# Performance work log

Hardware: AMD Instinct MI355X
Metric: run time of the kernel (lower is better)

The kernel has to match this reference:

```python
import jax, jax.numpy as jnp
import numpy as np

N_PROBLEMS = 20000
N_SKILLS = 1000
EMB_SIZE = 128
TIME_LOG = 5.0
B, L = 64, 1024


def setup_inputs() -> dict:
    key = jax.random.key(0)
    ks = jax.random.split(key, 10)
    skills = jax.random.randint(ks[0], (B, L), 0, N_SKILLS)
    problems = jax.random.randint(ks[1], (B, L), 0, N_PROBLEMS)
    labels = jax.random.randint(ks[2], (B, L), 0, 2)
    times = jnp.sort(jax.random.randint(ks[3], (B, L), 0, 1_000_000), axis=-1)
    inp = jnp.stack([skills, problems, labels, times], axis=1)  # [B,4,L]
    std = 0.01
    return {
        "input": inp,
        "problem_base": std * jax.random.normal(ks[4], (N_PROBLEMS, 1), jnp.float32),
        "skill_base": std * jax.random.normal(ks[5], (N_SKILLS, 1), jnp.float32),
        "alpha_inter": std * jax.random.normal(ks[6], (N_SKILLS * 2, EMB_SIZE), jnp.float32),
        "alpha_skill": std * jax.random.normal(ks[7], (N_SKILLS, EMB_SIZE), jnp.float32),
        "beta_inter": std * jax.random.normal(ks[8], (N_SKILLS * 2, EMB_SIZE), jnp.float32),
        "beta_skill": std * jax.random.normal(ks[9], (N_SKILLS, EMB_SIZE), jnp.float32),
    }


def reference(input, problem_base, skill_base, alpha_inter, alpha_skill, beta_inter, beta_skill):
    skills = input[:, 0]    # [B,L]
    problems = input[:, 1]
    labels = input[:, 2]
    times = input[:, 3]

    mask_labels = labels * (labels < 2).astype(labels.dtype)
    inters = skills + mask_labels * N_SKILLS  # [B,L] in [0, 2*N_SKILLS)

    # pairwise Hawkes excitation / decay scores: [B,L,L]
    alphas = jnp.einsum('bie,bje->bij', alpha_inter[inters], alpha_skill[skills])
    betas = jnp.einsum('bie,bje->bij', beta_inter[inters], beta_skill[skills])
    betas = jnp.clip(betas + 1.0, 0.0, 10.0)

    dt = jnp.abs(times[:, :, None] - times[:, None, :]).astype(jnp.float32)
    log_dt = jnp.log(dt + 1e-10) / np.log(TIME_LOG)

    cross_effects = alphas * jnp.exp(-betas * log_dt)

    seq_len = skills.shape[1]
    # keep strictly-upper-triangular entries (source i before target j)
    keep = jnp.triu(jnp.ones((seq_len, seq_len), dtype=bool), k=1)
    sum_t = jnp.where(keep[None], cross_effects, 0.0).sum(axis=-2)  # [B,L]

    problem_bias = problem_base[problems][..., 0]
    skill_bias = skill_base[skills][..., 0]
    return jax.nn.sigmoid(problem_bias + skill_bias + sum_t)
```

## Files before the change

### kernel.cpp

```cpp
#include <hip/hip_runtime.h>
#include <hip/hip_bf16.h>

#define NB   64
#define SL   1024
#define EMB  128
#define NSK  1000
#define TJ   64
#define TI   64
#define SB   136
#define NS   4

#define AI_OFF 0
#define BI_OFF 256000
#define AS_OFF 512000
#define BS_OFF 640000
#define TB_ELEMS 768000
#define ACC_BYTE_OFF (TB_ELEMS * 2)
#define ACC_ELEMS (NS * NB * SL)

using short8  = __attribute__((ext_vector_type(8))) short;
using floatx4 = __attribute__((ext_vector_type(4))) float;

__device__ inline unsigned cvt2(float x, float y) {
    float2 f; f.x = x; f.y = y;
    __hip_bfloat162 h = __float22bfloat162_rn(f);
    unsigned u; __builtin_memcpy(&u, &h, sizeof(u));
    return u;
}

extern "C" __global__ __launch_bounds__(256)
void cvt_tables(const float* __restrict__ ai, const float* __restrict__ bi,
                const float* __restrict__ as, const float* __restrict__ bs,
                unsigned short* __restrict__ dst)
{
    const int t = blockIdx.x * 256 + threadIdx.x;
    const long e = (long)t * 8;
    const float* src;
    if      (e < 256000) src = ai + e;
    else if (e < 512000) src = bi + (e - 256000);
    else if (e < 640000) src = as + (e - 512000);
    else                 src = bs + (e - 640000);
    float4 f0 = *(const float4*)src;
    float4 f1 = *(const float4*)(src + 4);
    uint4 pk;
    pk.x = cvt2(f0.x, f0.y); pk.y = cvt2(f0.z, f0.w);
    pk.z = cvt2(f1.x, f1.y); pk.w = cvt2(f1.z, f1.w);
    *(uint4*)(dst + e) = pk;
}

__device__ __noinline__ float fixup_pair(const float* __restrict__ air,
                                         const float* __restrict__ bir,
                                         const float* __restrict__ asr,
                                         const float* __restrict__ bsr) {
    float da = 0.f, db = 0.f;
    for (int k = 0; k < EMB; ++k) {
        da += air[k] * asr[k];
        db += bir[k] * bsr[k];
    }
    float beta = fminf(fmaxf(db + 1.f, 0.f), 10.f);
    return da * __expf(beta * 14.30676558073393f);
}

extern "C" __global__ __launch_bounds__(256)
void hawkes_main(const int*   __restrict__ inp,
                 const float* __restrict__ ainter,
                 const float* __restrict__ askill,
                 const float* __restrict__ bint,
                 const float* __restrict__ bsk,
                 const unsigned short* __restrict__ tb,
                 float*       __restrict__ acc)
{
    __shared__ unsigned short lA[2][TI][SB];

    const int bid  = blockIdx.x;
    const int b    = bid & (NB - 1);
    const int r    = bid >> 6;
    const int jt   = (SL / TJ - 1) - ((r >> 2) & 15);
    const int s    = r & 3;
    const int tid  = threadIdx.x;
    const int w    = tid >> 6;
    const int l    = tid & 63;
    const int quad = l >> 4;
    const int col  = l & 15;

    const int* __restrict__ binp = inp + b * 4 * SL;

    const int jlane = jt * TJ + w * 16 + col;
    const int sk_j  = binp[jlane];
    const int tj    = binp[3 * SL + jlane];
    const float* asr = askill + (long)sk_j * EMB;
    const float* bsr = bsk    + (long)sk_j * EMB;

    const unsigned short* asr16 = tb + AS_OFF + (long)sk_j * EMB;
    const unsigned short* bsr16 = tb + BS_OFF + (long)sk_j * EMB;
    short8 bfa[4], bfb[4];
#pragma unroll
    for (int ks = 0; ks < 4; ++ks) {
        int k0 = ks * 32 + quad * 8;
        bfa[ks] = *(const short8*)(asr16 + k0);
        bfb[ks] = *(const short8*)(bsr16 + k0);
    }

    float sum = 0.f;

    const int srow = tid >> 2;
    const int sq   = tid & 3;

    for (int it = s; it <= jt; it += NS) {
        const int itb = it * TI;

        {
            const int irow  = itb + srow;
            const int ski   = binp[irow];
            const int li    = binp[2 * SL + irow];
            const long intr = ski + (long)li * NSK;
            const unsigned short* sA = tb + AI_OFF + intr * EMB + sq * 32;
            const unsigned short* sBm = tb + BI_OFF + intr * EMB + sq * 32;
            uint4 a0 = *(const uint4*)(sA);
            uint4 a1 = *(const uint4*)(sA + 8);
            uint4 a2 = *(const uint4*)(sA + 16);
            uint4 a3 = *(const uint4*)(sA + 24);
            uint4 b0 = *(const uint4*)(sBm);
            uint4 b1 = *(const uint4*)(sBm + 8);
            uint4 b2 = *(const uint4*)(sBm + 16);
            uint4 b3 = *(const uint4*)(sBm + 24);
            unsigned short* dA = &lA[0][srow][sq * 32];
            unsigned short* dB = &lA[1][srow][sq * 32];
            *(uint4*)(dA)      = a0;
            *(uint4*)(dA + 8)  = a1;
            *(uint4*)(dA + 16) = a2;
            *(uint4*)(dA + 24) = a3;
            *(uint4*)(dB)      = b0;
            *(uint4*)(dB + 8)  = b1;
            *(uint4*)(dB + 16) = b2;
            *(uint4*)(dB + 24) = b3;
        }
        __syncthreads();

#pragma unroll
        for (int isub = 0; isub < 4; ++isub) {
            floatx4 acca = {0.f, 0.f, 0.f, 0.f};
            floatx4 accb = {0.f, 0.f, 0.f, 0.f};
#pragma unroll
            for (int ks = 0; ks < 4; ++ks) {
                int k0 = ks * 32 + quad * 8;
                short8 av = *(const short8*)&lA[0][isub * 16 + col][k0];
                short8 bv = *(const short8*)&lA[1][isub * 16 + col][k0];
                acca = __builtin_amdgcn_mfma_f32_16x16x32_bf16(av, bfa[ks], acca, 0, 0, 0);
                accb = __builtin_amdgcn_mfma_f32_16x16x32_bf16(bv, bfb[ks], accb, 0, 0, 0);
            }
            const int ibase = itb + isub * 16 + quad * 4;
            const int4 t4 = *(const int4*)(binp + 3 * SL + ibase);
#pragma unroll
            for (int rr = 0; rr < 4; ++rr) {
                const int iidx = ibase + rr;
                if (iidx < jlane) {
                    const int ti = (rr == 0) ? t4.x : (rr == 1) ? t4.y : (rr == 2) ? t4.z : t4.w;
                    const int dt = tj - ti;
                    if (dt != 0) {
                        float beta = fminf(fmaxf(accb[rr] + 1.f, 0.f), 10.f);
                        float lc   = __log2f((float)dt) * 0.43067655807339306f;
                        sum += acca[rr] * exp2f(-beta * lc);
                    } else {
                        const int ski   = binp[iidx];
                        const int li    = binp[2 * SL + iidx];
                        const long intr = ski + (long)li * NSK;
                        sum += fixup_pair(ainter + intr * EMB, bint + intr * EMB, asr, bsr);
                    }
                }
            }
        }
        __syncthreads();
    }

    sum += __shfl_xor(sum, 16, 64);
    sum += __shfl_xor(sum, 32, 64);

    if (quad == 0) {
        acc[(((long)s * NB + b) << 10) + jlane] = sum;
    }
}

extern "C" __global__ __launch_bounds__(256)
void hawkes_finalize(const int* __restrict__ inp, const float* __restrict__ pbase,
                     const float* __restrict__ sbase, const float* __restrict__ acc,
                     float* __restrict__ out)
{
    const int t = blockIdx.x * 256 + threadIdx.x;
    const int b = t >> 10, j = t & (SL - 1);
    const int* binp = inp + b * 4 * SL;
    float sum = acc[t] + acc[NB * SL + t] + acc[2 * NB * SL + t] + acc[3 * NB * SL + t];
    const float x = pbase[binp[SL + j]] + sbase[binp[j]] + sum;
    out[t] = 1.f / (1.f + __expf(-x));
}

extern "C" void kernel_launch(void* const* d_in, const int* in_sizes, int n_in,
                              void* d_out, int out_size, void* d_ws, size_t ws_size,
                              hipStream_t stream) {
    const int*   inp = (const int*)d_in[0];
    const float* pb  = (const float*)d_in[1];
    const float* sb  = (const float*)d_in[2];
    const float* ai  = (const float*)d_in[3];
    const float* as  = (const float*)d_in[4];
    const float* bi  = (const float*)d_in[5];
    const float* bs  = (const float*)d_in[6];

    unsigned short* tb  = (unsigned short*)d_ws;
    float*          acc = (float*)((char*)d_ws + ACC_BYTE_OFF);

    cvt_tables<<<dim3(96000 / 256), dim3(256), 0, stream>>>(ai, bi, as, bs, tb);
    hawkes_main<<<dim3(NB * (SL / TJ) * NS), dim3(256), 0, stream>>>(
        inp, ai, as, bi, bs, tb, acc);
    hawkes_finalize<<<dim3(NB * SL / 256), dim3(256), 0, stream>>>(
        inp, pb, sb, acc, (float*)d_out);
}
```

Baseline: 131.6 us.

## Swap loop order: stage i-tile once in LDS, stream 128-wide j-tiles

Each block now loads one 64-row i-tile of interaction embeddings into shared memory once and loops over 128-column j-tiles. Each wave handles two 16-column j groups, so every LDS read feeds four MFMAs instead of two. The loop-internal barriers and per-tile reloads go away. Partial sums are written per i-tile and reduced in a variable-length loop in the finalize kernel. In exchange, the j-side skill fragments are reloaded from global memory for every j-tile, register pressure rises, and the accumulator buffer grows to 16 slices.

```diff
diff --git a/kernel.cpp b/kernel.cpp
--- a/kernel.cpp
+++ b/kernel.cpp
@@ -5,10 +5,9 @@
 #define SL   1024
 #define EMB  128
 #define NSK  1000
-#define TJ   64
 #define TI   64
 #define SB   136
-#define NS   4
+#define NS   2
 
 #define AI_OFF 0
 #define BI_OFF 256000
@@ -16,10 +15,11 @@
 #define BS_OFF 640000
 #define TB_ELEMS 768000
 #define ACC_BYTE_OFF (TB_ELEMS * 2)
-#define ACC_ELEMS (NS * NB * SL)
 
 using short8  = __attribute__((ext_vector_type(8))) short;
 using floatx4 = __attribute__((ext_vector_type(4))) float;
+
+#define INV_LN5 0.6213349345596119f
 
 __device__ inline unsigned cvt2(float x, float y) {
     float2 f; f.x = x; f.y = y;
@@ -75,8 +75,8 @@
     const int bid  = blockIdx.x;
     const int b    = bid & (NB - 1);
     const int r    = bid >> 6;
-    const int jt   = (SL / TJ - 1) - ((r >> 2) & 15);
-    const int s    = r & 3;
+    const int it   = r >> 1;
+    const int s    = r & 1;
     const int tid  = threadIdx.x;
     const int w    = tid >> 6;
     const int l    = tid & 63;
@@ -84,100 +84,119 @@
     const int col  = l & 15;
 
     const int* __restrict__ binp = inp + b * 4 * SL;
-
-    const int jlane = jt * TJ + w * 16 + col;
-    const int sk_j  = binp[jlane];
-    const int tj    = binp[3 * SL + jlane];
-    const float* asr = askill + (long)sk_j * EMB;
-    const float* bsr = bsk    + (long)sk_j * EMB;
-
-    const unsigned short* asr16 = tb + AS_OFF + (long)sk_j * EMB;
-    const unsigned short* bsr16 = tb + BS_OFF + (long)sk_j * EMB;
-    short8 bfa[4], bfb[4];
-#pragma unroll
-    for (int ks = 0; ks < 4; ++ks) {
-        int k0 = ks * 32 + quad * 8;
-        bfa[ks] = *(const short8*)(asr16 + k0);
-        bfb[ks] = *(const short8*)(bsr16 + k0);
+    const int itb = it * TI;
+
+    {
+        const int srow  = tid >> 2;
+        const int sq    = tid & 3;
+        const int irow  = itb + srow;
+        const int ski   = binp[irow];
+        const int li    = binp[2 * SL + irow];
+        const long intr = ski + (long)li * NSK;
+        const unsigned short* sA  = tb + AI_OFF + intr * EMB + sq * 32;
+        const unsigned short* sBm = tb + BI_OFF + intr * EMB + sq * 32;
+        uint4 a0 = *(const uint4*)(sA);
+        uint4 a1 = *(const uint4*)(sA + 8);
+        uint4 a2 = *(const uint4*)(sA + 16);
+        uint4 a3 = *(const uint4*)(sA + 24);
+        uint4 b0 = *(const uint4*)(sBm);
+        uint4 b1 = *(const uint4*)(sBm + 8);
+        uint4 b2 = *(const uint4*)(sBm + 16);
+        uint4 b3 = *(const uint4*)(sBm + 24);
+        unsigned short* dA = &lA[0][srow][sq * 32];
+        unsigned short* dB = &lA[1][srow][sq * 32];
+        *(uint4*)(dA)      = a0; *(uint4*)(dA + 8)  = a1;
+        *(uint4*)(dA + 16) = a2; *(uint4*)(dA + 24) = a3;
+        *(uint4*)(dB)      = b0; *(uint4*)(dB + 8)  = b1;
+        *(uint4*)(dB + 16) = b2; *(uint4*)(dB + 24) = b3;
     }
 
-    float sum = 0.f;
-
-    const int srow = tid >> 2;
-    const int sq   = tid & 3;
-
-    for (int it = s; it <= jt; it += NS) {
-        const int itb = it * TI;
-
+    int4 t4s[4];
+#pragma unroll
+    for (int isub = 0; isub < 4; ++isub)
+        t4s[isub] = *(const int4*)(binp + 3 * SL + itb + isub * 16 + quad * 4);
+
+    __syncthreads();
+
+    const int jt_min = it >> 1;
+    for (int jt = jt_min; jt < 8; ++jt) {
+        if ((jt & 1) != s) continue;
+        const int jbase = jt * 128 + w * 32;
+        const int j0 = jbase + col;
+        const int j1 = jbase + 16 + col;
+        const int sk0 = binp[j0],        sk1 = binp[j1];
+        const int tj0 = binp[3*SL + j0], tj1 = binp[3*SL + j1];
+
+        short8 f00[4], f01[4], f10[4], f11[4];
         {
-            const int irow  = itb + srow;
-            const int ski   = binp[irow];
-            const int li    = binp[2 * SL + irow];
-            const long intr = ski + (long)li * NSK;
-            const unsigned short* sA = tb + AI_OFF + intr * EMB + sq * 32;
-            const unsigned short* sBm = tb + BI_OFF + intr * EMB + sq * 32;
-            uint4 a0 = *(const uint4*)(sA);
-            uint4 a1 = *(const uint4*)(sA + 8);
-            uint4 a2 = *(const uint4*)(sA + 16);
-            uint4 a3 = *(const uint4*)(sA + 24);
-            uint4 b0 = *(const uint4*)(sBm);
-            uint4 b1 = *(const uint4*)(sBm + 8);
-            uint4 b2 = *(const uint4*)(sBm + 16);
-            uint4 b3 = *(const uint4*)(sBm + 24);
-            unsigned short* dA = &lA[0][srow][sq * 32];
-            unsigned short* dB = &lA[1][srow][sq * 32];
-            *(uint4*)(dA)      = a0;
-            *(uint4*)(dA + 8)  = a1;
-            *(uint4*)(dA + 16) = a2;
-            *(uint4*)(dA + 24) = a3;
-            *(uint4*)(dB)      = b0;
-            *(uint4*)(dB + 8)  = b1;
-            *(uint4*)(dB + 16) = b2;
-            *(uint4*)(dB + 24) = b3;
+            const unsigned short* p00 = tb + AS_OFF + (long)sk0 * EMB + quad * 8;
+            const unsigned short* p01 = tb + BS_OFF + (long)sk0 * EMB + quad * 8;
+            const unsigned short* p10 = tb + AS_OFF + (long)sk1 * EMB + quad * 8;
+            const unsigned short* p11 = tb + BS_OFF + (long)sk1 * EMB + quad * 8;
+#pragma unroll
+            for (int ks = 0; ks < 4; ++ks) {
+                f00[ks] = *(const short8*)(p00 + ks * 32);
+                f01[ks] = *(const short8*)(p01 + ks * 32);
+                f10[ks] = *(const short8*)(p10 + ks * 32);
+                f11[ks] = *(const short8*)(p11 + ks * 32);
+            }
         }
-        __syncthreads();
-
+
+        float sum0 = 0.f, sum1 = 0.f;
 #pragma unroll
         for (int isub = 0; isub < 4; ++isub) {
-            floatx4 acca = {0.f, 0.f, 0.f, 0.f};
-            floatx4 accb = {0.f, 0.f, 0.f, 0.f};
+            floatx4 aa0 = {0.f,0.f,0.f,0.f}, aa1 = {0.f,0.f,0.f,0.f};
+            floatx4 bb0 = {0.f,0.f,0.f,0.f}, bb1 = {0.f,0.f,0.f,0.f};
 #pragma unroll
             for (int ks = 0; ks < 4; ++ks) {
-                int k0 = ks * 32 + quad * 8;
+                const int k0 = ks * 32 + quad * 8;
                 short8 av = *(const short8*)&lA[0][isub * 16 + col][k0];
                 short8 bv = *(const short8*)&lA[1][isub * 16 + col][k0];
-                acca = __builtin_amdgcn_mfma_f32_16x16x32_bf16(av, bfa[ks], acca, 0, 0, 0);
-                accb = __builtin_amdgcn_mfma_f32_16x16x32_bf16(bv, bfb[ks], accb, 0, 0, 0);
+                aa0 = __builtin_amdgcn_mfma_f32_16x16x32_bf16(av, f00[ks], aa0, 0, 0, 0);
+                aa1 = __builtin_amdgcn_mfma_f32_16x16x32_bf16(av, f10[ks], aa1, 0, 0, 0);
+                bb0 = __builtin_amdgcn_mfma_f32_16x16x32_bf16(bv, f01[ks], bb0, 0, 0, 0);
+                bb1 = __builtin_amdgcn_mfma_f32_16x16x32_bf16(bv, f11[ks], bb1, 0, 0, 0);
             }
             const int ibase = itb + isub * 16 + quad * 4;
-            const int4 t4 = *(const int4*)(binp + 3 * SL + ibase);
+            const int4 t4 = t4s[isub];
 #pragma unroll
             for (int rr = 0; rr < 4; ++rr) {
                 const int iidx = ibase + rr;
-                if (iidx < jlane) {
-                    const int ti = (rr == 0) ? t4.x : (rr == 1) ? t4.y : (rr == 2) ? t4.z : t4.w;
-                    const int dt = tj - ti;
+                const int ti = (rr == 0) ? t4.x : (rr == 1) ? t4.y : (rr == 2) ? t4.z : t4.w;
+                if (iidx < j0) {
+                    const int dt = tj0 - ti;
                     if (dt != 0) {
-                        float beta = fminf(fmaxf(accb[rr] + 1.f, 0.f), 10.f);
-                        float lc   = __log2f((float)dt) * 0.43067655807339306f;
-                        sum += acca[rr] * exp2f(-beta * lc);
+                        float beta = fminf(fmaxf(bb0[rr] + 1.f, 0.f), 10.f);
+                        sum0 += aa0[rr] * exp2f(-beta * (__log2f((float)dt) * INV_LN5));
                     } else {
-                        const int ski   = binp[iidx];
-                        const int li    = binp[2 * SL + iidx];
+                        const int ski = binp[iidx], li = binp[2*SL + iidx];
                         const long intr = ski + (long)li * NSK;
-                        sum += fixup_pair(ainter + intr * EMB, bint + intr * EMB, asr, bsr);
+                        sum0 += fixup_pair(ainter + intr * EMB, bint + intr * EMB,
+                                           askill + (long)sk0 * EMB, bsk + (long)sk0 * EMB);
+                    }
+                }
+                if (iidx < j1) {
+                    const int dt = tj1 - ti;
+                    if (dt != 0) {
+                        float beta = fminf(fmaxf(bb1[rr] + 1.f, 0.f), 10.f);
+                        sum1 += aa1[rr] * exp2f(-beta * (__log2f((float)dt) * INV_LN5));
+                    } else {
+                        const int ski = binp[iidx], li = binp[2*SL + iidx];
+                        const long intr = ski + (long)li * NSK;
+                        sum1 += fixup_pair(ainter + intr * EMB, bint + intr * EMB,
+                                           askill + (long)sk1 * EMB, bsk + (long)sk1 * EMB);
                     }
                 }
             }
         }
-        __syncthreads();
-    }
-
-    sum += __shfl_xor(sum, 16, 64);
-    sum += __shfl_xor(sum, 32, 64);
-
-    if (quad == 0) {
-        acc[(((long)s * NB + b) << 10) + jlane] = sum;
+
+        sum0 += __shfl_xor(sum0, 16, 64); sum0 += __shfl_xor(sum0, 32, 64);
+        sum1 += __shfl_xor(sum1, 16, 64); sum1 += __shfl_xor(sum1, 32, 64);
+        if (quad == 0) {
+            float* as_ = acc + (((long)it * NB + b) << 10);
+            as_[j0] = sum0;
+            as_[j1] = sum1;
+        }
     }
 }
 
@@ -189,7 +208,10 @@
     const int t = blockIdx.x * 256 + threadIdx.x;
     const int b = t >> 10, j = t & (SL - 1);
     const int* binp = inp + b * 4 * SL;
-    float sum = acc[t] + acc[NB * SL + t] + acc[2 * NB * SL + t] + acc[3 * NB * SL + t];
+    const int itmax = min(15, 2 * (j >> 7) + 1);
+    float sum = 0.f;
+    for (int it = 0; it <= itmax; ++it)
+        sum += acc[(((long)it * NB + b) << 10) + j];
     const float x = pbase[binp[SL + j]] + sbase[binp[j]] + sum;
     out[t] = 1.f / (1.f + __expf(-x));
 }
@@ -209,7 +231,7 @@
     float*          acc = (float*)((char*)d_ws + ACC_BYTE_OFF);
 
     cvt_tables<<<dim3(96000 / 256), dim3(256), 0, stream>>>(ai, bi, as, bs, tb);
-    hawkes_main<<<dim3(NB * (SL / TJ) * NS), dim3(256), 0, stream>>>(
+    hawkes_main<<<dim3(NB * 16 * NS), dim3(256), 0, stream>>>(
         inp, ai, as, bi, bs, tb, acc);
     hawkes_finalize<<<dim3(NB * SL / 256), dim3(256), 0, stream>>>(
         inp, pb, sb, acc, (float*)d_out);
```

After: 181.8 us. 1.38x slower.

## Prefetch next i-tile into registers, move equal-time fixups to finalize, halve split

Applied to the files above, without the earlier changes.

The main loop now issues the global loads for the next i-tile into registers while the current tile is computed, giving a software-pipelined LDS fill. The per-pair causal mask and the dt==0 fixup branch leave the inner loop: dt<=0 gives exp2(-inf)=0 and contributes nothing, while equal-timestamp pairs are handled by a scan in the finalize kernel. The i-range split drops from 4 to 2 and launch bounds request 4 blocks per CU. Fewer blocks means less parallelism but also fewer partial sums to reduce, and the finalize kernel gains a serial loop over equal-time neighbours.

```diff
diff --git a/kernel.cpp b/kernel.cpp
--- a/kernel.cpp
+++ b/kernel.cpp
@@ -5,10 +5,9 @@
 #define SL   1024
 #define EMB  128
 #define NSK  1000
-#define TJ   64
 #define TI   64
 #define SB   136
-#define NS   4
+#define NS   2
 
 #define AI_OFF 0
 #define BI_OFF 256000
@@ -16,10 +15,11 @@
 #define BS_OFF 640000
 #define TB_ELEMS 768000
 #define ACC_BYTE_OFF (TB_ELEMS * 2)
-#define ACC_ELEMS (NS * NB * SL)
 
 using short8  = __attribute__((ext_vector_type(8))) short;
 using floatx4 = __attribute__((ext_vector_type(4))) float;
+
+#define INV_LOG2_5 0.43067655807339306f
 
 __device__ inline unsigned cvt2(float x, float y) {
     float2 f; f.x = x; f.y = y;
@@ -48,10 +48,10 @@
     *(uint4*)(dst + e) = pk;
 }
 
-__device__ __noinline__ float fixup_pair(const float* __restrict__ air,
-                                         const float* __restrict__ bir,
-                                         const float* __restrict__ asr,
-                                         const float* __restrict__ bsr) {
+__device__ float fixup_pair(const float* __restrict__ air,
+                            const float* __restrict__ bir,
+                            const float* __restrict__ asr,
+                            const float* __restrict__ bsr) {
     float da = 0.f, db = 0.f;
     for (int k = 0; k < EMB; ++k) {
         da += air[k] * asr[k];
@@ -61,12 +61,8 @@
     return da * __expf(beta * 14.30676558073393f);
 }
 
-extern "C" __global__ __launch_bounds__(256)
+extern "C" __global__ __launch_bounds__(256, 4)
 void hawkes_main(const int*   __restrict__ inp,
-                 const float* __restrict__ ainter,
-                 const float* __restrict__ askill,
-                 const float* __restrict__ bint,
-                 const float* __restrict__ bsk,
                  const unsigned short* __restrict__ tb,
                  float*       __restrict__ acc)
 {
@@ -75,8 +71,8 @@
     const int bid  = blockIdx.x;
     const int b    = bid & (NB - 1);
     const int r    = bid >> 6;
-    const int jt   = (SL / TJ - 1) - ((r >> 2) & 15);
-    const int s    = r & 3;
+    const int jt   = 15 - (r >> 1);
+    const int s    = r & 1;
     const int tid  = threadIdx.x;
     const int w    = tid >> 6;
     const int l    = tid & 63;
@@ -85,92 +81,88 @@
 
     const int* __restrict__ binp = inp + b * 4 * SL;
 
-    const int jlane = jt * TJ + w * 16 + col;
+    const int jlane = jt * TI + w * 16 + col;
     const int sk_j  = binp[jlane];
     const int tj    = binp[3 * SL + jlane];
-    const float* asr = askill + (long)sk_j * EMB;
-    const float* bsr = bsk    + (long)sk_j * EMB;
-
-    const unsigned short* asr16 = tb + AS_OFF + (long)sk_j * EMB;
-    const unsigned short* bsr16 = tb + BS_OFF + (long)sk_j * EMB;
+
+    const unsigned short* asr16 = tb + AS_OFF + (long)sk_j * EMB + quad * 8;
+    const unsigned short* bsr16 = tb + BS_OFF + (long)sk_j * EMB + quad * 8;
     short8 bfa[4], bfb[4];
 #pragma unroll
     for (int ks = 0; ks < 4; ++ks) {
-        int k0 = ks * 32 + quad * 8;
-        bfa[ks] = *(const short8*)(asr16 + k0);
-        bfb[ks] = *(const short8*)(bsr16 + k0);
-    }
-
-    float sum = 0.f;
+        bfa[ks] = *(const short8*)(asr16 + ks * 32);
+        bfb[ks] = *(const short8*)(bsr16 + ks * 32);
+    }
 
     const int srow = tid >> 2;
     const int sq   = tid & 3;
-
-    for (int it = s; it <= jt; it += NS) {
-        const int itb = it * TI;
-
+    unsigned short* dA = &lA[0][srow][sq * 32];
+    unsigned short* dB = &lA[1][srow][sq * 32];
+
+    float sum = 0.f;
+
+    if (s <= jt) {
+        uint4 pa0, pa1, pa2, pa3, pb0, pb1, pb2, pb3;
         {
-            const int irow  = itb + srow;
+            const int irow  = s * TI + srow;
             const int ski   = binp[irow];
             const int li    = binp[2 * SL + irow];
             const long intr = ski + (long)li * NSK;
-            const unsigned short* sA = tb + AI_OFF + intr * EMB + sq * 32;
+            const unsigned short* sA  = tb + AI_OFF + intr * EMB + sq * 32;
             const unsigned short* sBm = tb + BI_OFF + intr * EMB + sq * 32;
-            uint4 a0 = *(const uint4*)(sA);
-            uint4 a1 = *(const uint4*)(sA + 8);
-            uint4 a2 = *(const uint4*)(sA + 16);
-            uint4 a3 = *(const uint4*)(sA + 24);
-            uint4 b0 = *(const uint4*)(sBm);
-            uint4 b1 = *(const uint4*)(sBm + 8);
-            uint4 b2 = *(const uint4*)(sBm + 16);
-            uint4 b3 = *(const uint4*)(sBm + 24);
-            unsigned short* dA = &lA[0][srow][sq * 32];
-            unsigned short* dB = &lA[1][srow][sq * 32];
-            *(uint4*)(dA)      = a0;
-            *(uint4*)(dA + 8)  = a1;
-            *(uint4*)(dA + 16) = a2;
-            *(uint4*)(dA + 24) = a3;
-            *(uint4*)(dB)      = b0;
-            *(uint4*)(dB + 8)  = b1;
-            *(uint4*)(dB + 16) = b2;
-            *(uint4*)(dB + 24) = b3;
+            pa0 = *(const uint4*)(sA);      pa1 = *(const uint4*)(sA + 8);
+            pa2 = *(const uint4*)(sA + 16); pa3 = *(const uint4*)(sA + 24);
+            pb0 = *(const uint4*)(sBm);     pb1 = *(const uint4*)(sBm + 8);
+            pb2 = *(const uint4*)(sBm + 16);pb3 = *(const uint4*)(sBm + 24);
         }
-        __syncthreads();
-
-#pragma unroll
-        for (int isub = 0; isub < 4; ++isub) {
-            floatx4 acca = {0.f, 0.f, 0.f, 0.f};
-            floatx4 accb = {0.f, 0.f, 0.f, 0.f};
-#pragma unroll
-            for (int ks = 0; ks < 4; ++ks) {
-                int k0 = ks * 32 + quad * 8;
-                short8 av = *(const short8*)&lA[0][isub * 16 + col][k0];
-                short8 bv = *(const short8*)&lA[1][isub * 16 + col][k0];
-                acca = __builtin_amdgcn_mfma_f32_16x16x32_bf16(av, bfa[ks], acca, 0, 0, 0);
-                accb = __builtin_amdgcn_mfma_f32_16x16x32_bf16(bv, bfb[ks], accb, 0, 0, 0);
+
+        for (int it = s; it <= jt; it += NS) {
+            __syncthreads();
+            *(uint4*)(dA)      = pa0; *(uint4*)(dA + 8)  = pa1;
+            *(uint4*)(dA + 16) = pa2; *(uint4*)(dA + 24) = pa3;
+            *(uint4*)(dB)      = pb0; *(uint4*)(dB + 8)  = pb1;
+            *(uint4*)(dB + 16) = pb2; *(uint4*)(dB + 24) = pb3;
+
+            if (it + NS <= jt) {
+                const int irow  = (it + NS) * TI + srow;
+                const int ski   = binp[irow];
+                const int li    = binp[2 * SL + irow];
+                const long intr = ski + (long)li * NSK;
+                const unsigned short* sA  = tb + AI_OFF + intr * EMB + sq * 32;
+                const unsigned short* sBm = tb + BI_OFF + intr * EMB + sq * 32;
+                pa0 = *(const uint4*)(sA);      pa1 = *(const uint4*)(sA + 8);
+                pa2 = *(const uint4*)(sA + 16); pa3 = *(const uint4*)(sA + 24);
+                pb0 = *(const uint4*)(sBm);     pb1 = *(const uint4*)(sBm + 8);
+                pb2 = *(const uint4*)(sBm + 16);pb3 = *(const uint4*)(sBm + 24);
             }
-            const int ibase = itb + isub * 16 + quad * 4;
-            const int4 t4 = *(const int4*)(binp + 3 * SL + ibase);
-#pragma unroll
-            for (int rr = 0; rr < 4; ++rr) {
-                const int iidx = ibase + rr;
-                if (iidx < jlane) {
+            __syncthreads();
+
+            const int itb = it * TI;
+#pragma unroll
+            for (int isub = 0; isub < 4; ++isub) {
+                floatx4 aa = {0.f, 0.f, 0.f, 0.f};
+                floatx4 bb = {0.f, 0.f, 0.f, 0.f};
+#pragma unroll
+                for (int ks = 0; ks < 4; ++ks) {
+                    const int k0 = ks * 32 + quad * 8;
+                    short8 av = *(const short8*)&lA[0][isub * 16 + col][k0];
+                    short8 bv = *(const short8*)&lA[1][isub * 16 + col][k0];
+                    aa = __builtin_amdgcn_mfma_f32_16x16x32_bf16(av, bfa[ks], aa, 0, 0, 0);
+                    bb = __builtin_amdgcn_mfma_f32_16x16x32_bf16(bv, bfb[ks], bb, 0, 0, 0);
+                }
+                const int ibase = itb + isub * 16 + quad * 4;
+                const int4 t4 = *(const int4*)(binp + 3 * SL + ibase);
+#pragma unroll
+                for (int rr = 0; rr < 4; ++rr) {
                     const int ti = (rr == 0) ? t4.x : (rr == 1) ? t4.y : (rr == 2) ? t4.z : t4.w;
                     const int dt = tj - ti;
-                    if (dt != 0) {
-                        float beta = fminf(fmaxf(accb[rr] + 1.f, 0.f), 10.f);
-                        float lc   = __log2f((float)dt) * 0.43067655807339306f;
-                        sum += acca[rr] * exp2f(-beta * lc);
-                    } else {
-                        const int ski   = binp[iidx];
-                        const int li    = binp[2 * SL + iidx];
-                        const long intr = ski + (long)li * NSK;
-                        sum += fixup_pair(ainter + intr * EMB, bint + intr * EMB, asr, bsr);
-                    }
+                    float lc  = __log2f((float)dt);
+                    float nb  = fminf(fmaxf(bb[rr] + 1.f, 0.f), 10.f) * (-INV_LOG2_5);
+                    float arg = (dt > 0) ? nb * lc : -__builtin_inff();
+                    sum += aa[rr] * exp2f(arg);
                 }
             }
         }
-        __syncthreads();
     }
 
     sum += __shfl_xor(sum, 16, 64);
@@ -183,14 +175,27 @@
 
 extern "C" __global__ __launch_bounds__(256)
 void hawkes_finalize(const int* __restrict__ inp, const float* __restrict__ pbase,
-                     const float* __restrict__ sbase, const float* __restrict__ acc,
-                     float* __restrict__ out)
+                     const float* __restrict__ sbase,
+                     const float* __restrict__ ai, const float* __restrict__ as,
+                     const float* __restrict__ bi, const float* __restrict__ bs,
+                     const float* __restrict__ acc, float* __restrict__ out)
 {
     const int t = blockIdx.x * 256 + threadIdx.x;
     const int b = t >> 10, j = t & (SL - 1);
     const int* binp = inp + b * 4 * SL;
-    float sum = acc[t] + acc[NB * SL + t] + acc[2 * NB * SL + t] + acc[3 * NB * SL + t];
-    const float x = pbase[binp[SL + j]] + sbase[binp[j]] + sum;
+    const int tj   = binp[3 * SL + j];
+    const int sk_j = binp[j];
+
+    float corr = 0.f;
+    for (int i = j - 1; i >= 0 && binp[3 * SL + i] == tj; --i) {
+        const int ski = binp[i], li = binp[2 * SL + i];
+        const long intr = ski + (long)li * NSK;
+        corr += fixup_pair(ai + intr * EMB, bi + intr * EMB,
+                           as + (long)sk_j * EMB, bs + (long)sk_j * EMB);
+    }
+
+    float sum = acc[t] + acc[NB * SL + t] + corr;
+    const float x = pbase[binp[SL + j]] + sbase[sk_j] + sum;
     out[t] = 1.f / (1.f + __expf(-x));
 }
 
@@ -209,8 +214,7 @@
     float*          acc = (float*)((char*)d_ws + ACC_BYTE_OFF);
 
     cvt_tables<<<dim3(96000 / 256), dim3(256), 0, stream>>>(ai, bi, as, bs, tb);
-    hawkes_main<<<dim3(NB * (SL / TJ) * NS), dim3(256), 0, stream>>>(
-        inp, ai, as, bi, bs, tb, acc);
+    hawkes_main<<<dim3(NB * 16 * NS), dim3(256), 0, stream>>>(inp, tb, acc);
     hawkes_finalize<<<dim3(NB * SL / 256), dim3(256), 0, stream>>>(
-        inp, pb, sb, acc, (float*)d_out);
-}
+        inp, pb, sb, ai, as, bi, bs, acc, (float*)d_out);
+}
```

Measured after the change: 115.1 us. -12.6%, faster.
